# Kernel tuning notes

Hardware: AMD Instinct MI355X
Metric: run time of the kernel (lower is better)

Reference implementation:

```python
import jax, jax.numpy as jnp
from jax import lax
import numpy as np

IMG = 2048.0            # square image size (W=H)
STRIDES = [32, 64, 128]
FEATS = [64, 32, 16]    # IMG / stride
NUM_CLASSES = 80
BATCH = 8
SCORE_THRESH = 0.2
NMS_THRESH = 0.6
TOPK = 1000             # topk_candidates per level
DETS = 100              # detections_per_img


def make_anchors(fs, stride):
    # square anchors of size==stride centered on the feature grid (AnchorGenerator with ratio 1.0)
    c = (jnp.arange(fs, dtype=jnp.float32) + 0.5) * stride
    cy, cx = jnp.meshgrid(c, c, indexing='ij')
    cx, cy = cx.reshape(-1), cy.reshape(-1)
    h = stride / 2.0
    return jnp.stack([cx - h, cy - h, cx + h, cy + h], axis=1)


def setup_inputs() -> dict:
    key = jax.random.key(0)
    inp = {}
    for i, (fs, s) in enumerate(zip(FEATS, STRIDES)):
        hw = fs * fs
        key, k1, k2, k3 = jax.random.split(key, 4)
        inp[f'cls{i}'] = jax.random.normal(k1, (BATCH, hw, NUM_CLASSES), jnp.float32)
        inp[f'reg{i}'] = jax.random.uniform(k2, (BATCH, hw, 4), jnp.float32)
        inp[f'ctr{i}'] = jax.random.normal(k3, (BATCH, hw), jnp.float32)
        inp[f'anc{i}'] = make_anchors(fs, float(s))
    return inp


def _decode(rel, boxes):
    # BoxLinearCoder.decode_single with normalize_by_size=True
    cx = 0.5 * (boxes[:, 0] + boxes[:, 2])
    cy = 0.5 * (boxes[:, 1] + boxes[:, 3])
    w = boxes[:, 2] - boxes[:, 0]
    h = boxes[:, 3] - boxes[:, 1]
    rel = rel * jnp.stack([w, h, w, h], axis=1)
    return jnp.stack([cx - rel[:, 0], cy - rel[:, 1], cx + rel[:, 2], cy + rel[:, 3]], axis=1)


def _iou(b):
    # torchvision box_iou on a single set of boxes [N,4] -> [N,N]
    area = (b[:, 2] - b[:, 0]) * (b[:, 3] - b[:, 1])
    lt = jnp.maximum(b[:, None, :2], b[None, :, :2])
    rb = jnp.minimum(b[:, None, 2:], b[None, :, 2:])
    wh = jnp.clip(rb - lt, 0.0)
    inter = wh[..., 0] * wh[..., 1]
    return inter / (area[:, None] + area[None, :] - inter)


def _greedy_keep(iou):
    # classic greedy NMS on score-sorted boxes: suppress j>i with iou>thresh if i kept
    n = iou.shape[0]
    idx = jnp.arange(n)
    def body(i, keep):
        supp = keep[i] & (iou[i] > NMS_THRESH) & (idx > i)
        return keep & ~supp
    return lax.fori_loop(0, n, body, jnp.ones((n,), bool))


def _per_image(cls_l, reg_l, ctr_l, anc_l):
    boxes, scores, labels = [], [], []
    for cls, reg, ctr, anc in zip(cls_l, reg_l, ctr_l, anc_l):
        hw, c = cls.shape
        # scores = sqrt(sigmoid(cls) * sigmoid(ctrness)) flattened over anchors*classes
        sc = jnp.sqrt(jax.nn.sigmoid(cls) * jax.nn.sigmoid(ctr)[:, None]).reshape(-1)
        sc = jnp.where(sc > SCORE_THRESH, sc, -1.0)  # score threshold as mask (static shapes)
        ts, ti = lax.top_k(sc, TOPK)                 # per-level top-k candidates
        aidx = ti // c
        lab = ti % c
        b = jnp.clip(_decode(reg[aidx], anc[aidx]), 0.0, IMG)  # decode + clip to image
        boxes.append(b); scores.append(ts); labels.append(lab)
    boxes = jnp.concatenate(boxes)    # [3*TOPK, 4]
    scores = jnp.concatenate(scores)  # [3*TOPK]
    labels = jnp.concatenate(labels)  # [3*TOPK]
    n = scores.shape[0]
    # batched_nms via per-class coordinate offsets
    off = labels.astype(boxes.dtype) * (IMG + 1.0)
    ss, oi = lax.top_k(scores, n)     # sort candidates by score desc
    bs = boxes[oi] + off[oi][:, None]
    keep = lax.stop_gradient(_greedy_keep(_iou(bs)))
    fsc = jnp.where(keep & (ss > 0), ss, -1.0)
    fs, fi = lax.top_k(fsc, DETS)     # keep detections_per_img; score==-1 marks padding
    return boxes[oi][fi], fs, labels[oi][fi]


def reference(cls0, cls1, cls2, reg0, reg1, reg2, ctr0, ctr1, ctr2, anc0, anc1, anc2):
    f = jax.vmap(lambda c0, c1, c2, r0, r1, r2, t0, t1, t2: _per_image(
        [c0, c1, c2], [r0, r1, r2], [t0, t1, t2], [anc0, anc1, anc2]))
    return f(cls0, cls1, cls2, reg0, reg1, reg2, ctr0, ctr1, ctr2)
```

## Files before the change

### kernel.cpp

```cpp
#include <hip/hip_runtime.h>

#define NCLS  80
#define TOPK  1000
#define NLVL  3
#define NIMG  8
#define NCAND 3000
#define DETS  100
#define CAP   2048
#define HBINS 4096
#define NHBLK 16
#define NCBLK 64
#define QBASE 0x3F800000u
#define QMAX  0x41C80000u
#define IMGSZ 2048.0f


__device__ __forceinline__ float sigm(float x) {
    if (x >= 0.f) return 1.f / (1.f + expf(-x));
    float e = expf(x);
    return e / (1.f + e);
}

__device__ __forceinline__ unsigned int qbits(float ea, float t1) {
    return __float_as_uint(__fmul_rn(__fadd_rn(1.f, ea), t1));
}

__device__ __forceinline__ void bitonic_desc(unsigned long long* s, int N) {
    for (int k = 2; k <= N; k <<= 1) {
        for (int j = k >> 1; j > 0; j >>= 1) {
            __syncthreads();
            for (int i = threadIdx.x; i < N; i += blockDim.x) {
                int ixj = i ^ j;
                if (ixj > i) {
                    unsigned long long a = s[i], b = s[ixj];
                    bool up = ((i & k) == 0);
                    if (up ? (a < b) : (a > b)) { s[i] = b; s[ixj] = a; }
                }
            }
        }
    }
    __syncthreads();
}

__device__ __forceinline__ void lvl_select(int level,
    const float* c0, const float* c1, const float* c2,
    const float* t0, const float* t1, const float* t2,
    const float** cls, const float** ctr, int* hw) {
    if (level == 0)      { *cls = c0; *ctr = t0; *hw = 4096; }
    else if (level == 1) { *cls = c1; *ctr = t1; *hw = 1024; }
    else                 { *cls = c2; *ctr = t2; *hw = 256; }
}


__global__ void k_hist(const float* c0, const float* c1, const float* c2,
                       const float* t0, const float* t1, const float* t2,
                       unsigned int* parts) {
    int level = blockIdx.z, img = blockIdx.y;
    const float* cls; const float* ctr; int hw;
    lvl_select(level, c0, c1, c2, t0, t1, t2, &cls, &ctr, &hw);
    int n4 = hw * (NCLS / 4);
    const float4* cl4 = (const float4*)(cls + (size_t)img * hw * NCLS);
    const float* ct = ctr + (size_t)img * hw;
    __shared__ unsigned int h[HBINS];
    for (int i = threadIdx.x; i < HBINS; i += 256) h[i] = 0;
    __syncthreads();
    for (int i = blockIdx.x * 256 + threadIdx.x; i < n4; i += NHBLK * 256) {
        float4 v = cl4[i];
        int a = i / (NCLS / 4);
        float eb = expf(-ct[a]);
        float t1 = __fadd_rn(1.f, eb);
        #pragma unroll
        for (int k = 0; k < 4; ++k) {
            float x = (k == 0) ? v.x : (k == 1) ? v.y : (k == 2) ? v.z : v.w;
            unsigned int qb = qbits(expf(-x), t1);
            if (qb < QMAX) {
                unsigned int bin = (qb - QBASE) >> 13;
                if (bin > HBINS - 1) bin = HBINS - 1;
                atomicAdd(&h[bin], 1u);
            }
        }
    }
    __syncthreads();
    unsigned int* P = parts + ((size_t)((img * NLVL + level) * NHBLK + blockIdx.x)) * HBINS;
    for (int i = threadIdx.x; i < HBINS; i += 256) P[i] = h[i];
}


__global__ void k_find(const unsigned int* parts, unsigned int* vcut) {
    int pair = blockIdx.x;
    int tid = threadIdx.x;
    __shared__ unsigned int hb[HBINS];
    __shared__ unsigned int segsum[256];
    __shared__ unsigned int pref[256];
    unsigned int acc[HBINS / 256];
    #pragma unroll
    for (int j = 0; j < HBINS / 256; ++j) acc[j] = 0;
    for (int blk = 0; blk < NHBLK; ++blk) {
        const unsigned int* P = parts + ((size_t)(pair * NHBLK + blk)) * HBINS;
        #pragma unroll
        for (int j = 0; j < HBINS / 256; ++j) acc[j] += P[tid + 256 * j];
    }
    #pragma unroll
    for (int j = 0; j < HBINS / 256; ++j) hb[tid + 256 * j] = acc[j];
    __syncthreads();
    unsigned int seg = 0;
    #pragma unroll
    for (int j = 0; j < 16; ++j) seg += hb[16 * tid + j];
    segsum[tid] = seg;
    pref[tid] = seg;
    __syncthreads();
    for (int off = 1; off < 256; off <<= 1) {
        unsigned int v = (tid >= off) ? pref[tid - off] : 0u;
        __syncthreads();
        pref[tid] += v;
        __syncthreads();
    }
    unsigned int incl = pref[tid];
    unsigned int excl = incl - seg;
    if (excl < (unsigned int)TOPK && incl >= (unsigned int)TOPK) {
        unsigned int cum = excl; int B = HBINS - 1;
        for (int b = 16 * tid; b < 16 * tid + 16; ++b) {
            cum += hb[b];
            if (cum >= (unsigned int)TOPK) { B = b; break; }
        }
        vcut[pair] = (B >= HBINS - 1) ? QMAX : (QBASE + ((unsigned int)(B + 1) << 13));
    }
    if (tid == 255 && pref[255] < (unsigned int)TOPK)
        vcut[pair] = QMAX;
}


__global__ void k_collect(const float* c0, const float* c1, const float* c2,
                          const float* t0, const float* t1, const float* t2,
                          const unsigned int* vcut, unsigned int* counters,
                          unsigned long long* buf) {
    int level = blockIdx.z, img = blockIdx.y;
    const float* cls; const float* ctr; int hw;
    lvl_select(level, c0, c1, c2, t0, t1, t2, &cls, &ctr, &hw);
    int n4 = hw * (NCLS / 4);
    int pair = img * NLVL + level;
    const float4* cl4 = (const float4*)(cls + (size_t)img * hw * NCLS);
    const float* ct = ctr + (size_t)img * hw;
    unsigned int V = vcut[pair];
    __shared__ unsigned long long sbuf[2048];
    __shared__ unsigned int scnt;
    __shared__ unsigned int sbase;
    if (threadIdx.x == 0) scnt = 0;
    __syncthreads();
    for (int i = blockIdx.x * 256 + threadIdx.x; i < n4; i += NCBLK * 256) {
        float4 v = cl4[i];
        int a = i / (NCLS / 4);
        float cta = ct[a];
        float eb = expf(-cta);
        float t1 = __fadd_rn(1.f, eb);
        #pragma unroll
        for (int k = 0; k < 4; ++k) {
            float x = (k == 0) ? v.x : (k == 1) ? v.y : (k == 2) ? v.z : v.w;
            unsigned int qb = qbits(expf(-x), t1);
            if (qb < V) {
                float s = sqrtf(sigm(x) * sigm(cta));
                unsigned int e = (unsigned int)(4 * i + k);
                unsigned int slot = atomicAdd(&scnt, 1u);
                if (slot < 2048)
                    sbuf[slot] = ((unsigned long long)__float_as_uint(s) << 32) | (~e);
            }
        }
    }
    __syncthreads();
    unsigned int cl_n = scnt; if (cl_n > 2048) cl_n = 2048;
    if (threadIdx.x == 0)
        sbase = atomicAdd(&counters[pair * 16], cl_n);
    __syncthreads();
    unsigned int base = sbase;
    for (unsigned int idx = threadIdx.x; idx < cl_n; idx += 256) {
        unsigned int g = base + idx;
        if (g < CAP) buf[(size_t)pair * CAP + g] = sbuf[idx];
    }
}


__global__ void __launch_bounds__(1024)
k_sort_pairs(const unsigned long long* buf, const unsigned int* counters,
             const float* r0, const float* r1, const float* r2,
             const float* a0, const float* a1, const float* a2,
             float* cand_box, int* cand_lab, unsigned long long* gkey) {
    int pair = blockIdx.x;
    int img = pair / NLVL, level = pair % NLVL;
    __shared__ unsigned long long s[CAP];
    int cnt = (int)counters[pair * 16]; if (cnt > CAP) cnt = CAP;
    for (int i = threadIdx.x; i < CAP; i += blockDim.x)
        s[i] = (i < cnt) ? buf[(size_t)pair * CAP + i] : 0ull;
    bitonic_desc(s, CAP);
    const float* reg; const float* anc; int hw;
    if (level == 0)      { reg = r0; anc = a0; hw = 4096; }
    else if (level == 1) { reg = r1; anc = a1; hw = 1024; }
    else                 { reg = r2; anc = a2; hw = 256; }
    const float* rg = reg + (size_t)img * hw * 4;
    for (int r = threadIdx.x; r < TOPK; r += blockDim.x) {
        unsigned long long key = s[r];
        int cpos = level * TOPK + r;
        size_t o = (size_t)img * NCAND + cpos;
        float b0 = 0, b1 = 0, b2 = 0, b3 = 0; int lab = 0; unsigned int bits = 0;
        if (key != 0ull) {
            bits = (unsigned int)(key >> 32);
            unsigned int idx = ~((unsigned int)key);
            int a = (int)(idx / NCLS); lab = (int)(idx % NCLS);
            float ax1 = anc[a * 4 + 0], ay1 = anc[a * 4 + 1];
            float ax2 = anc[a * 4 + 2], ay2 = anc[a * 4 + 3];
            float cx = 0.5f * (ax1 + ax2), cy = 0.5f * (ay1 + ay2);
            float w = ax2 - ax1, h = ay2 - ay1;
            float e0 = rg[a * 4 + 0] * w, e1 = rg[a * 4 + 1] * h;
            float e2 = rg[a * 4 + 2] * w, e3 = rg[a * 4 + 3] * h;
            b0 = fminf(fmaxf(cx - e0, 0.f), IMGSZ);
            b1 = fminf(fmaxf(cy - e1, 0.f), IMGSZ);
            b2 = fminf(fmaxf(cx + e2, 0.f), IMGSZ);
            b3 = fminf(fmaxf(cy + e3, 0.f), IMGSZ);
        }
        cand_box[o * 4 + 0] = b0; cand_box[o * 4 + 1] = b1;
        cand_box[o * 4 + 2] = b2; cand_box[o * 4 + 3] = b3;
        cand_lab[o] = lab;
        gkey[o] = ((unsigned long long)bits << 32) | (unsigned int)(~((unsigned int)cpos));
    }
}


__global__ void __launch_bounds__(1024)
k_merge_nms(const unsigned long long* gkey, const float* cand_box, const int* cand_lab,
            float* out) {
    int img = blockIdx.x;
    int tid = threadIdx.x;
    __shared__ unsigned long long A[TOPK], B[TOPK], C[TOPK];
    __shared__ unsigned long long M[2 * TOPK];
    __shared__ unsigned long long S[NCAND];
    __shared__ float4 wbox[1024];
    __shared__ int    wlab[1024];
    __shared__ float4 kb[DETS]; __shared__ float ks[DETS]; __shared__ int kl[DETS];
    __shared__ float4 rb[DETS]; __shared__ int rl[DETS];

    const unsigned long long* G = gkey + (size_t)img * NCAND;
    for (int i = tid; i < TOPK; i += 1024) { A[i] = G[i]; B[i] = G[TOPK + i]; C[i] = G[2 * TOPK + i]; }
    __syncthreads();

    for (int k = tid; k < 2 * TOPK; k += 1024) {
        int lo = max(0, k - TOPK), hi = min(k, TOPK);
        while (lo < hi) {
            int mid = (lo + hi) >> 1;
            if (A[mid] > B[k - mid - 1]) lo = mid + 1; else hi = mid;
        }
        int i = lo, j = k - lo;
        unsigned long long av = (i < TOPK) ? A[i] : 0ull;
        unsigned long long bv = (j < TOPK) ? B[j] : 0ull;
        M[k] = (av > bv) ? av : bv;
    }
    __syncthreads();
    for (int k = tid; k < NCAND; k += 1024) {
        int lo = max(0, k - TOPK), hi = min(k, 2 * TOPK);
        while (lo < hi) {
            int mid = (lo + hi) >> 1;
            if (M[mid] > C[k - mid - 1]) lo = mid + 1; else hi = mid;
        }
        int i = lo, j = k - lo;
        unsigned long long mv = (i < 2 * TOPK) ? M[i] : 0ull;
        unsigned long long cv = (j < TOPK) ? C[j] : 0ull;
        S[k] = (mv > cv) ? mv : cv;
    }
    __syncthreads();

    const float4* CB4 = (const float4*)cand_box + (size_t)img * NCAND;
    const int* CL = cand_lab + (size_t)img * NCAND;
    {
        unsigned int pos = ~((unsigned int)S[tid]);
        wbox[tid] = CB4[pos];
        wlab[tid] = CL[pos];
    }
    __syncthreads();

    if (tid >= 64) return;
    int lane = tid;

    float aX1 = 0, aY1 = 0, aX2 = 0, aY2 = 0, aAR = 0;
    float bX1 = 0, bY1 = 0, bX2 = 0, bY2 = 0, bAR = 0;
    int kept = 0, ring = 0;

    for (int r = 0; r < NCAND && kept < DETS; ++r) {
        unsigned long long key = S[r];
        unsigned int bits = (unsigned int)(key >> 32);
        float4 bx; int lb;
        if (r < 1024) { bx = wbox[r]; lb = wlab[r]; }
        else { unsigned int pos = ~((unsigned int)key); bx = CB4[pos]; lb = CL[pos]; }

        if (bits != 0u) {
            float sc = __uint_as_float(bits);
            float off = (float)lb * (IMGSZ + 1.0f);
            float ox1 = bx.x + off, oy1 = bx.y + off;
            float ox2 = bx.z + off, oy2 = bx.w + off;
            float car = (ox2 - ox1) * (oy2 - oy1);
            bool sup = false;
            if (lane < kept) {
                float lx = fmaxf(aX1, ox1), ly = fmaxf(aY1, oy1);
                float rx = fminf(aX2, ox2), ry = fminf(aY2, oy2);
                float w = fmaxf(rx - lx, 0.f), h = fmaxf(ry - ly, 0.f);
                float inter = w * h;
                float iou = inter / (aAR + car - inter);
                sup = iou > 0.6f;
            }
            if (lane + 64 < kept) {
                float lx = fmaxf(bX1, ox1), ly = fmaxf(bY1, oy1);
                float rx = fminf(bX2, ox2), ry = fminf(bY2, oy2);
                float w = fmaxf(rx - lx, 0.f), h = fmaxf(ry - ly, 0.f);
                float inter = w * h;
                float iou = inter / (bAR + car - inter);
                sup = sup || (iou > 0.6f);
            }
            unsigned long long m = __ballot(sup);
            if (m == 0ull) {
                if (kept < 64) {
                    if (lane == kept) { aX1 = ox1; aY1 = oy1; aX2 = ox2; aY2 = oy2; aAR = car; }
                } else {
                    if (lane == kept - 64) { bX1 = ox1; bY1 = oy1; bX2 = ox2; bY2 = oy2; bAR = car; }
                }
                if (lane == 0) { kb[kept] = bx; ks[kept] = sc; kl[kept] = lb; }
                kept++;
            } else if (ring < DETS) {
                if (lane == 0) { rb[ring] = bx; rl[ring] = lb; }
                ring++;
            }
        } else {
            if (ring < DETS) {
                if (lane == 0) { rb[ring] = bx; rl[ring] = lb; }
                ring++;
            }
            if (ring >= DETS) break;
        }
    }

    for (int k = lane; k < DETS; k += 64) {
        float4 bxo; float scv; int lv;
        if (k < kept) { bxo = kb[k]; scv = ks[k]; lv = kl[k]; }
        else { int q = k - kept; bxo = rb[q]; scv = -1.0f; lv = rl[q]; }
        float* ob = out + ((size_t)img * DETS + k) * 4;
        ob[0] = bxo.x; ob[1] = bxo.y; ob[2] = bxo.z; ob[3] = bxo.w;
        out[NIMG * DETS * 4 + img * DETS + k] = scv;
        out[NIMG * DETS * 5 + img * DETS + k] = (float)lv;
    }
}


extern "C" void kernel_launch(void* const* d_in, const int* in_sizes, int n_in,
                              void* d_out, int out_size, void* d_ws, size_t ws_size,
                              hipStream_t stream) {
    (void)in_sizes; (void)n_in; (void)out_size; (void)ws_size;
    const float* cls0 = (const float*)d_in[0];
    const float* reg0 = (const float*)d_in[1];
    const float* ctr0 = (const float*)d_in[2];
    const float* anc0 = (const float*)d_in[3];
    const float* cls1 = (const float*)d_in[4];
    const float* reg1 = (const float*)d_in[5];
    const float* ctr1 = (const float*)d_in[6];
    const float* anc1 = (const float*)d_in[7];
    const float* cls2 = (const float*)d_in[8];
    const float* reg2 = (const float*)d_in[9];
    const float* ctr2 = (const float*)d_in[10];
    const float* anc2 = (const float*)d_in[11];
    float* out = (float*)d_out;
    char* ws = (char*)d_ws;

    const size_t OFF_PARTS = 0;
    const size_t OFF_CNT   = 6291456;
    const size_t ZERO_OFF  = 6291456;
    const size_t ZERO_B    = 1536;
    const size_t OFF_VCUT  = 6292992;
    const size_t OFF_BUF   = 6293120;
    const size_t OFF_CBOX  = 6686336;
    const size_t OFF_CLAB  = 7070336;
    const size_t OFF_GKEY  = 7166336;

    unsigned int* parts = (unsigned int*)(ws + OFF_PARTS);
    unsigned int* cnt   = (unsigned int*)(ws + OFF_CNT);
    unsigned int* vcut  = (unsigned int*)(ws + OFF_VCUT);
    unsigned long long* buf  = (unsigned long long*)(ws + OFF_BUF);
    float* cand_box = (float*)(ws + OFF_CBOX);
    int*   cand_lab = (int*)(ws + OFF_CLAB);
    unsigned long long* gkey = (unsigned long long*)(ws + OFF_GKEY);

    hipMemsetAsync(ws + ZERO_OFF, 0, ZERO_B, stream);

    k_hist<<<dim3(NHBLK, NIMG, NLVL), 256, 0, stream>>>(cls0, cls1, cls2, ctr0, ctr1, ctr2, parts);
    k_find<<<24, 256, 0, stream>>>(parts, vcut);
    k_collect<<<dim3(NCBLK, NIMG, NLVL), 256, 0, stream>>>(cls0, cls1, cls2, ctr0, ctr1, ctr2,
                                                           vcut, cnt, buf);
    k_sort_pairs<<<24, 1024, 0, stream>>>(buf, cnt, reg0, reg1, reg2, anc0, anc1, anc2,
                                          cand_box, cand_lab, gkey);
    k_merge_nms<<<NIMG, 1024, 0, stream>>>(gkey, cand_box, cand_lab, out);
}
```

Before: 197.7 us.

## Process NMS candidates in 64-wide chunks with intra-chunk IoU bitmask resolution

Replaces the one-candidate-per-iteration greedy NMS loop with a chunked scheme. Each wave iteration loads 64 consecutive sorted candidates and tests each against all kept boxes in parallel. It builds a pairwise suppression bitmask within the chunk and resolves greedy order with ballots, which cuts the number of serial wave iterations. The shared-memory gather is reduced to 512 entries, and the trailing zero-score padding is filled 64 at a time. The cost is extra per-lane IoU work against every kept box and a more complex rank/ring bookkeeping that could diverge from reference ordering.

```diff
diff --git a/kernel.cpp b/kernel.cpp
--- a/kernel.cpp
+++ b/kernel.cpp
@@ -10,6 +10,7 @@
 #define HBINS 4096
 #define NHBLK 16
 #define NCBLK 64
+#define GATH  512
 #define QBASE 0x3F800000u
 #define QMAX  0x41C80000u
 #define IMGSZ 2048.0f
@@ -232,8 +233,10 @@
     __shared__ unsigned long long A[TOPK], B[TOPK], C[TOPK];
     __shared__ unsigned long long M[2 * TOPK];
     __shared__ unsigned long long S[NCAND];
-    __shared__ float4 wbox[1024];
-    __shared__ int    wlab[1024];
+    __shared__ float4 wbox[GATH];
+    __shared__ int    wlab[GATH];
+    __shared__ float4 sbx[64]; __shared__ float sar[64];
+    __shared__ float4 koff[DETS]; __shared__ float karr[DETS];
     __shared__ float4 kb[DETS]; __shared__ float ks[DETS]; __shared__ int kl[DETS];
     __shared__ float4 rb[DETS]; __shared__ int rl[DETS];
 
@@ -268,70 +271,105 @@
 
     const float4* CB4 = (const float4*)cand_box + (size_t)img * NCAND;
     const int* CL = cand_lab + (size_t)img * NCAND;
-    {
+    if (tid < GATH) {
         unsigned int pos = ~((unsigned int)S[tid]);
-        wbox[tid] = CB4[pos];
-        wlab[tid] = CL[pos];
+        float4 b4 = make_float4(0.f, 0.f, 0.f, 0.f); int lbv = 0;
+        if (pos < NCAND) { b4 = CB4[pos]; lbv = CL[pos]; }
+        wbox[tid] = b4; wlab[tid] = lbv;
     }
     __syncthreads();
 
     if (tid >= 64) return;
     int lane = tid;
-
-    float aX1 = 0, aY1 = 0, aX2 = 0, aY2 = 0, aAR = 0;
-    float bX1 = 0, bY1 = 0, bX2 = 0, bY2 = 0, bAR = 0;
-    int kept = 0, ring = 0;
-
-    for (int r = 0; r < NCAND && kept < DETS; ++r) {
-        unsigned long long key = S[r];
+    unsigned long long lmask_lt = (lane == 0) ? 0ull : (~0ull >> (64 - lane));
+
+    int kept = 0, ring = 0, r = 0;
+
+    while (kept < DETS && r < NCAND) {
+        int rank = r + lane;
+        unsigned long long key = (rank < NCAND) ? S[rank] : 0ull;
         unsigned int bits = (unsigned int)(key >> 32);
-        float4 bx; int lb;
-        if (r < 1024) { bx = wbox[r]; lb = wlab[r]; }
-        else { unsigned int pos = ~((unsigned int)key); bx = CB4[pos]; lb = CL[pos]; }
-
-        if (bits != 0u) {
-            float sc = __uint_as_float(bits);
-            float off = (float)lb * (IMGSZ + 1.0f);
-            float ox1 = bx.x + off, oy1 = bx.y + off;
-            float ox2 = bx.z + off, oy2 = bx.w + off;
-            float car = (ox2 - ox1) * (oy2 - oy1);
-            bool sup = false;
-            if (lane < kept) {
-                float lx = fmaxf(aX1, ox1), ly = fmaxf(aY1, oy1);
-                float rx = fminf(aX2, ox2), ry = fminf(aY2, oy2);
-                float w = fmaxf(rx - lx, 0.f), h = fmaxf(ry - ly, 0.f);
-                float inter = w * h;
-                float iou = inter / (aAR + car - inter);
-                sup = iou > 0.6f;
+        unsigned long long pm = __ballot(bits != 0u);
+        int npos = (pm == ~0ull) ? 64 : (int)__builtin_ctzll(~pm);
+        if (npos == 0) break;
+
+        float4 bx = make_float4(0.f, 0.f, 0.f, 0.f); int lb = 0;
+        if (lane < npos) {
+            unsigned int pos = ~((unsigned int)key);
+            if (rank < GATH) { bx = wbox[rank]; lb = wlab[rank]; }
+            else if (pos < NCAND) { bx = CB4[pos]; lb = CL[pos]; }
+        }
+        float off = (float)lb * (IMGSZ + 1.0f);
+        float ox1 = bx.x + off, oy1 = bx.y + off;
+        float ox2 = bx.z + off, oy2 = bx.w + off;
+        float car = (ox2 - ox1) * (oy2 - oy1);
+        sbx[lane] = make_float4(ox1, oy1, ox2, oy2);
+        sar[lane] = car;
+
+        bool supk = false;
+        for (int k2 = 0; k2 < kept; ++k2) {
+            float4 kk = koff[k2]; float ka = karr[k2];
+            float lx = fmaxf(kk.x, ox1), ly = fmaxf(kk.y, oy1);
+            float rx = fminf(kk.z, ox2), ry = fminf(kk.w, oy2);
+            float w = fmaxf(rx - lx, 0.f), h = fmaxf(ry - ly, 0.f);
+            float inter = w * h;
+            supk = supk || (inter / (ka + car - inter) > 0.6f);
+        }
+        unsigned long long col = 0ull;
+        for (int i = 0; i < npos; ++i) {
+            float4 c = sbx[i]; float ca = sar[i];
+            float lx = fmaxf(c.x, ox1), ly = fmaxf(c.y, oy1);
+            float rx = fminf(c.z, ox2), ry = fminf(c.w, oy2);
+            float w = fmaxf(rx - lx, 0.f), h = fmaxf(ry - ly, 0.f);
+            float inter = w * h;
+            if ((inter / (ca + car - inter) > 0.6f) && (i < lane)) col |= (1ull << i);
+        }
+        unsigned long long undecided = __ballot((lane < npos) && !supk);
+        unsigned long long aliveSel = 0ull;
+        int capleft = DETS - kept;
+        int lastSlot = npos - 1;
+        while (undecided) {
+            int i = (int)__builtin_ctzll(undecided);
+            aliveSel |= (1ull << i);
+            undecided &= ~(1ull << i);
+            if (--capleft == 0) { lastSlot = i; break; }
+            unsigned long long row = __ballot(((col >> i) & 1ull) != 0ull);
+            undecided &= ~row;
+        }
+        unsigned long long region = (lastSlot >= 63) ? ~0ull : ((1ull << (lastSlot + 1)) - 1ull);
+        region &= (npos >= 64) ? ~0ull : ((1ull << npos) - 1ull);
+        unsigned long long rejm = region & ~aliveSel;
+
+        if ((aliveSel >> lane) & 1ull) {
+            int ki = kept + (int)__popcll(aliveSel & lmask_lt);
+            koff[ki] = make_float4(ox1, oy1, ox2, oy2); karr[ki] = car;
+            kb[ki] = bx; ks[ki] = __uint_as_float(bits); kl[ki] = lb;
+        }
+        if ((rejm >> lane) & 1ull) {
+            int ri = ring + (int)__popcll(rejm & lmask_lt);
+            if (ri < DETS) { rb[ri] = bx; rl[ri] = lb; }
+        }
+        kept += (int)__popcll(aliveSel);
+        ring += (int)__popcll(rejm);
+        r += lastSlot + 1;
+    }
+
+    while (kept < DETS && ring < DETS && r < NCAND) {
+        int rank = r + lane;
+        if (rank < NCAND) {
+            int ri = ring + lane;
+            if (ri < DETS) {
+                unsigned long long key = S[rank];
+                unsigned int pos = ~((unsigned int)key);
+                float4 bx = make_float4(0.f, 0.f, 0.f, 0.f); int lb = 0;
+                if (rank < GATH) { bx = wbox[rank]; lb = wlab[rank]; }
+                else if (pos < NCAND) { bx = CB4[pos]; lb = CL[pos]; }
+                rb[ri] = bx; rl[ri] = lb;
             }
-            if (lane + 64 < kept) {
-                float lx = fmaxf(bX1, ox1), ly = fmaxf(bY1, oy1);
-                float rx = fminf(bX2, ox2), ry = fminf(bY2, oy2);
-                float w = fmaxf(rx - lx, 0.f), h = fmaxf(ry - ly, 0.f);
-                float inter = w * h;
-                float iou = inter / (bAR + car - inter);
-                sup = sup || (iou > 0.6f);
-            }
-            unsigned long long m = __ballot(sup);
-            if (m == 0ull) {
-                if (kept < 64) {
-                    if (lane == kept) { aX1 = ox1; aY1 = oy1; aX2 = ox2; aY2 = oy2; aAR = car; }
-                } else {
-                    if (lane == kept - 64) { bX1 = ox1; bY1 = oy1; bX2 = ox2; bY2 = oy2; bAR = car; }
-                }
-                if (lane == 0) { kb[kept] = bx; ks[kept] = sc; kl[kept] = lb; }
-                kept++;
-            } else if (ring < DETS) {
-                if (lane == 0) { rb[ring] = bx; rl[ring] = lb; }
-                ring++;
-            }
-        } else {
-            if (ring < DETS) {
-                if (lane == 0) { rb[ring] = bx; rl[ring] = lb; }
-                ring++;
-            }
-            if (ring >= DETS) break;
-        }
+        }
+        int take = NCAND - r; if (take > 64) take = 64;
+        ring += take;
+        r += 64;
     }
 
     for (int k = lane; k < DETS; k += 64) {
```

New measurement: 178.9 us. -9.5%, faster.
